# Kernel optimization log

Measured on AMD Instinct MI355X. Metric: run time of the kernel, lower is better.

The kernel has to match this reference:

```python
import jax, jax.numpy as jnp
import numpy as np

DIM = 256
NUM_HEADS = 8
HEAD_DIM = DIM // NUM_HEADS  # 32
SCALE = HEAD_DIM ** (-0.5)


def _conv1x1(x, w, b):
    # x: [B,C,H,W], w: [O,C,1,1], b: [O]
    return jnp.einsum('bchw,oc->bohw', x, w[:, :, 0, 0]) + b[None, :, None, None]


def _dwconv3x3(x, w, b):
    # depthwise conv, groups=C, padding=1 (SAME)
    y = jax.lax.conv_general_dilated(
        x, w, window_strides=(1, 1), padding='SAME',
        feature_group_count=x.shape[1],
        dimension_numbers=('NCHW', 'OIHW', 'NCHW'))
    return y + b[None, :, None, None]


def setup_inputs() -> dict:
    key = jax.random.key(0)
    ks = jax.random.split(key, 9)
    s = 0.05
    return {
        'x': jax.random.normal(ks[0], (4, DIM, 48, 48), jnp.float32),
        'w_qk': jax.random.normal(ks[1], (2 * DIM, DIM, 1, 1), jnp.float32) * s,
        'b_qk': jax.random.normal(ks[2], (2 * DIM,), jnp.float32) * s,
        'w_v': jax.random.normal(ks[3], (DIM, DIM, 1, 1), jnp.float32) * s,
        'b_v': jax.random.normal(ks[4], (DIM,), jnp.float32) * s,
        'w_pe': jax.random.normal(ks[5], (DIM, 1, 3, 3), jnp.float32) * s,
        'b_pe': jax.random.normal(ks[6], (DIM,), jnp.float32) * s,
        'w_proj': jax.random.normal(ks[7], (DIM, DIM, 1, 1), jnp.float32) * s,
        'b_proj': jax.random.normal(ks[8], (DIM,), jnp.float32) * s,
    }


def reference(x, w_qk, b_qk, w_v, b_v, w_pe, b_pe, w_proj, b_proj):
    B, C, H, W = x.shape
    N = H * W
    h, d = NUM_HEADS, HEAD_DIM

    qk = _conv1x1(x, w_qk, b_qk).reshape(B, h, 2 * d, N)
    v4 = _conv1x1(x, w_v, b_v)                # [B,C,H,W]
    pe = _dwconv3x3(v4, w_pe, b_pe)           # [B,C,H,W]
    v = v4.reshape(B, h, d, N)

    q, k = qk[:, :, :d, :], qk[:, :, d:, :]   # [B,h,d,N] each
    attn = jnp.einsum('bhdi,bhdj->bhij', q, k) * SCALE  # [B,h,N,N]
    attn = jax.nn.softmax(attn, axis=-1)
    out = jnp.einsum('bhdj,bhij->bhdi', v, attn)        # [B,h,d,N]
    out = out.reshape(B, C, H, W)

    return _conv1x1(out + pe, w_proj, b_proj)
```

## Files before the change

### kernel.cpp

```cpp
#include <hip/hip_runtime.h>
#include <hip/hip_bf16.h>

#define NPIX 2304
#define HW 48
#define CDIM 256
#define NHEADS 8
#define HD 32
#define SCALE_CONST 0.17677669529663687f
#define LOG2E 1.4426950408889634f

typedef __attribute__((ext_vector_type(8))) short  short8v;
typedef __attribute__((ext_vector_type(4))) short  short4v;
typedef __attribute__((ext_vector_type(4))) float  floatx4;

__device__ inline short f2bf(float f) {
    unsigned u = __builtin_bit_cast(unsigned, f);
    u += 0x7FFFu + ((u >> 16) & 1u);
    return (short)(u >> 16);
}
__device__ inline float bf2f(unsigned short us) {
    return __builtin_bit_cast(float, (unsigned)us << 16);
}
__device__ inline float fexp2(float x) {
    return __builtin_amdgcn_exp2f(x);
}

__global__ __launch_bounds__(256) void prep_kernel(
    const float* __restrict__ x,
    short* __restrict__ XT,
    const float* __restrict__ wqk, const float* __restrict__ wv,
    const float* __restrict__ wp,
    short* __restrict__ wqkb, short* __restrict__ wvb, short* __restrict__ wpb)
{
    const int bx = blockIdx.x;
    const int t = threadIdx.x;
    if (bx >= 576) {
        int tid = (bx - 576) * 256 + t;
        for (int idx = tid; idx < 262144; idx += 16384) {
            if (idx < 131072)       wqkb[idx] = f2bf(wqk[idx]);
            else if (idx < 196608)  wvb[idx - 131072] = f2bf(wv[idx - 131072]);
            else                    wpb[idx - 196608] = f2bf(wp[idx - 196608]);
        }
        return;
    }
    __shared__ float sT[64][65];
    const int nt = bx % 36, ct = (bx / 36) & 3, b = bx / 144;
    const int c0 = ct * 64, n0 = nt * 64;
    const float* sp = x + ((size_t)b * 256 + c0) * NPIX + n0;
    const int cl = t >> 6, n = t & 63;
#pragma unroll
    for (int it = 0; it < 16; ++it) {
        int c = it * 4 + cl;
        sT[n][c] = sp[(size_t)c * NPIX + n];
    }
    __syncthreads();
    const int nr = t >> 2, q = t & 3;
    short out[16];
#pragma unroll
    for (int j = 0; j < 16; ++j) out[j] = f2bf(sT[nr][q * 16 + j]);
    short* dp = XT + ((size_t)b * NPIX + n0 + nr) * 256 + c0 + q * 16;
    *(int4*)dp = *(int4*)out;
    *(int4*)(dp + 8) = *(int4*)(out + 8);
}

#define XROW 528

__device__ inline void stage_xt_tile(const short* __restrict__ src_base,
                                     char* __restrict__ sX, int t)
{
    const short* src = src_base + (size_t)(t >> 3) * 256 + (t & 7) * 32;
    char* dst = sX + (t >> 3) * XROW + (t & 7) * 64;
#pragma unroll
    for (int rr = 0; rr < 2; ++rr) {
        const short* s = src + rr * 32 * 256;
        char* d = dst + rr * 32 * XROW;
        *(int4*)d        = *(const int4*)s;
        *(int4*)(d + 16) = *(const int4*)(s + 8);
        *(int4*)(d + 32) = *(const int4*)(s + 16);
        *(int4*)(d + 48) = *(const int4*)(s + 24);
    }
}

__global__ __launch_bounds__(256) void conv_qkv_mfma(
    const short* __restrict__ Wqk,
    const short* __restrict__ Wv,
    const float* __restrict__ bqk,
    const float* __restrict__ bv,
    const short* __restrict__ XT,
    short* __restrict__ QT,
    short* __restrict__ KT,
    short* __restrict__ VB)
{
    __shared__ __align__(16) char sX[64 * XROW];
    const int n0 = blockIdx.x * 64;
    const int og = blockIdx.y;
    const int b  = blockIdx.z;
    const int t = threadIdx.x, lane = t & 63, w = t >> 6;
    const int l15 = lane & 15, quad = lane >> 4;

    stage_xt_tile(XT + ((size_t)b * NPIX + n0) * 256, sX, t);
    __syncthreads();

    const bool isV = (og >= 8);
    const short* Wb = isV ? Wv + (size_t)((og - 8) * 64 + w * 16 + l15) * CDIM
                          : Wqk + (size_t)(og * 64 + w * 16 + l15) * CDIM;

    floatx4 acc[4];
#pragma unroll
    for (int ib = 0; ib < 4; ++ib) acc[ib] = (floatx4){0.f, 0.f, 0.f, 0.f};

#pragma unroll
    for (int s = 0; s < 8; ++s) {
        short8v af = *(const short8v*)(Wb + s * 32 + quad * 8);
#pragma unroll
        for (int ib = 0; ib < 4; ++ib) {
            short8v bf = *(const short8v*)(sX + (ib * 16 + l15) * XROW + s * 64 + quad * 16);
            acc[ib] = __builtin_amdgcn_mfma_f32_16x16x32_bf16(af, bf, acc[ib], 0, 0, 0);
        }
    }

    if (!isV) {
        const bool isQ = (w < 2);
        const int d0 = (w & 1) * 16 + quad * 4;
        const float scl = isQ ? SCALE_CONST * LOG2E : 1.0f;
        float bvv[4];
#pragma unroll
        for (int r = 0; r < 4; ++r) bvv[r] = bqk[og * 64 + w * 16 + quad * 4 + r];
        short* base = (isQ ? QT : KT) + (size_t)(b * 8 + og) * NPIX * HD;
#pragma unroll
        for (int ib = 0; ib < 4; ++ib) {
            short pb[4];
#pragma unroll
            for (int r = 0; r < 4; ++r) pb[r] = f2bf((acc[ib][r] + bvv[r]) * scl);
            *(short4v*)(base + (size_t)(n0 + ib * 16 + l15) * HD + d0) = *(short4v*)pb;
        }
    } else {
        const int o0 = (og - 8) * 64 + w * 16 + quad * 4;
#pragma unroll
        for (int r = 0; r < 4; ++r) {
            int o = o0 + r;
            float bb = bv[o];
#pragma unroll
            for (int ib = 0; ib < 4; ++ib) {
                VB[((size_t)b * 256 + o) * NPIX + n0 + ib * 16 + l15] = f2bf(acc[ib][r] + bb);
            }
        }
    }
}

__global__ __launch_bounds__(256) void dwconv3x3_kernel(
    const short* __restrict__ X,
    const float* __restrict__ Wp,
    const float* __restrict__ bp,
    float* __restrict__ Y)
{
    __shared__ short spl[NPIX];
    const int bc = blockIdx.x;
    const int c = bc & 255;
    const short* xp = X + (size_t)bc * NPIX;
    const int t = threadIdx.x;
    for (int idx = t; idx < NPIX / 8; idx += 256)
        *(int4*)&spl[idx * 8] = *(const int4*)(xp + idx * 8);
    float w[9];
#pragma unroll
    for (int i = 0; i < 9; ++i) w[i] = Wp[c * 9 + i];
    const float bb = bp[c];
    __syncthreads();

    for (int p = t; p < NPIX; p += 256) {
        int i = p / HW, j = p % HW;
        float acc = bb;
#pragma unroll
        for (int di = -1; di <= 1; ++di) {
            int ii = i + di;
            if (ii < 0 || ii >= HW) continue;
#pragma unroll
            for (int dj = -1; dj <= 1; ++dj) {
                int jj = j + dj;
                if (jj < 0 || jj >= HW) continue;
                acc += bf2f((unsigned short)spl[ii * HW + jj]) * w[(di + 1) * 3 + (dj + 1)];
            }
        }
        Y[(size_t)bc * NPIX + p] = acc;
    }
}

#define SK0 0
#define SK1 5120
#define SV0 10240
#define SV1 14848
#define SP0 19456
#define FL_SMEM 28672

__global__ __launch_bounds__(256) void flash_attn_mfma(
    const short* __restrict__ QT,
    const short* __restrict__ KT,
    const short* __restrict__ VB,
    const float* __restrict__ PE,
    short* __restrict__ ST)
{
    __shared__ __align__(16) char smem[FL_SMEM];

    const int i0 = blockIdx.x * 64;
    const int bh = blockIdx.y;
    const int b  = bh >> 3, hh = bh & 7;

    const short* KTp = KT + (size_t)bh * NPIX * HD;
    const short* Vp  = VB + (size_t)(b * 256 + hh * HD) * NPIX;

    const int t    = threadIdx.x;
    const int lane = t & 63;
    const int w    = t >> 6;
    const int l15  = lane & 15;
    const int quad = lane >> 4;

    const short8v qfrag = *(const short8v*)(
        QT + ((size_t)bh * NPIX + i0 + w * 16 + l15) * HD + quad * 8);

    char* const sPw = smem + SP0 + w * (16 * 144);

    float m_i = -1e30f, l_i = 0.f;
    floatx4 oacc[2];
    oacc[0] = (floatx4){0.f, 0.f, 0.f, 0.f};
    oacc[1] = (floatx4){0.f, 0.f, 0.f, 0.f};

    const short* ksrc = KTp + (size_t)(t >> 2) * HD + (t & 3) * 8;
    const short* vsrc = Vp + (size_t)(t >> 3) * NPIX + (t & 7) * 8;
    const int koff = (t >> 2) * 80 + (t & 3) * 16;
    const int voff = (t >> 3) * 144 + (t & 7) * 16;

    int4 kst = *(const int4*)ksrc;
    int4 vst = *(const int4*)vsrc;

    for (int it = 0; it < 36; ++it) {
        char* bufK = smem + ((it & 1) ? SK1 : SK0);
        char* bufV = smem + ((it & 1) ? SV1 : SV0);
        *(int4*)(bufK + koff) = kst;
        *(int4*)(bufV + voff) = vst;
        if (it + 1 < 36) {
            kst = *(const int4*)(ksrc + (size_t)(it + 1) * 64 * HD);
            vst = *(const int4*)(vsrc + (it + 1) * 64);
        }
        __syncthreads();

        floatx4 sacc[4];
#pragma unroll
        for (int jb = 0; jb < 4; ++jb) {
            short8v af = *(const short8v*)(bufK + (jb * 16 + l15) * 80 + quad * 16);
            sacc[jb] = __builtin_amdgcn_mfma_f32_16x16x32_bf16(
                af, qfrag, (floatx4){0.f, 0.f, 0.f, 0.f}, 0, 0, 0);
        }

        float mx = sacc[0][0];
#pragma unroll
        for (int jb = 0; jb < 4; ++jb)
#pragma unroll
            for (int r = 0; r < 4; ++r) mx = fmaxf(mx, sacc[jb][r]);
        mx = fmaxf(mx, __shfl_xor(mx, 16));
        mx = fmaxf(mx, __shfl_xor(mx, 32));

        float mn = fmaxf(m_i, mx);
        float alpha = fexp2(m_i - mn);
        m_i = mn;

        float s = 0.f;
#pragma unroll
        for (int jb = 0; jb < 4; ++jb) {
            short pb[4];
#pragma unroll
            for (int r = 0; r < 4; ++r) {
                float e = fexp2(sacc[jb][r] - mn);
                s += e;
                pb[r] = f2bf(e);
            }
            *(short4v*)(sPw + l15 * 144 + (jb * 16 + quad * 4) * 2) = *(short4v*)pb;
        }
        s += __shfl_xor(s, 16);
        s += __shfl_xor(s, 32);
        l_i = alpha * l_i + s;

#pragma unroll
        for (int r = 0; r < 4; ++r) { oacc[0][r] *= alpha; oacc[1][r] *= alpha; }

#pragma unroll
        for (int ks = 0; ks < 2; ++ks) {
            short8v pf = *(const short8v*)(sPw + l15 * 144 + ks * 64 + quad * 16);
#pragma unroll
            for (int db = 0; db < 2; ++db) {
                short8v vf = *(const short8v*)(bufV + (db * 16 + l15) * 144 + ks * 64 + quad * 16);
                oacc[db] = __builtin_amdgcn_mfma_f32_16x16x32_bf16(vf, pf, oacc[db], 0, 0, 0);
            }
        }
    }

    const float invl = 1.0f / l_i;
    const int i = i0 + w * 16 + l15;
    const float* PEp = PE + ((size_t)b * 256 + hh * HD) * NPIX + i;
    short* stp = ST + ((size_t)b * NPIX + i) * 256 + hh * HD;
#pragma unroll
    for (int db = 0; db < 2; ++db) {
        short pb[4];
#pragma unroll
        for (int r = 0; r < 4; ++r) {
            int d = db * 16 + quad * 4 + r;
            float v = oacc[db][r] * invl + PEp[(size_t)d * NPIX];
            pb[r] = f2bf(v);
        }
        *(short4v*)(stp + db * 16 + quad * 4) = *(short4v*)pb;
    }
}

__global__ __launch_bounds__(256) void conv_proj_mfma(
    const short* __restrict__ Wb,
    const float* __restrict__ bias,
    const short* __restrict__ ST,
    float* __restrict__ out)
{
    __shared__ __align__(16) char sX[64 * XROW];
    const int n0 = blockIdx.x * 64;
    const int og = blockIdx.y;
    const int b  = blockIdx.z;
    const int t = threadIdx.x, lane = t & 63, w = t >> 6;
    const int l15 = lane & 15, quad = lane >> 4;

    stage_xt_tile(ST + ((size_t)b * NPIX + n0) * 256, sX, t);
    __syncthreads();

    const short* Arow = Wb + (size_t)(og * 64 + w * 16 + l15) * CDIM;
    floatx4 acc[4];
#pragma unroll
    for (int ib = 0; ib < 4; ++ib) acc[ib] = (floatx4){0.f, 0.f, 0.f, 0.f};
#pragma unroll
    for (int s = 0; s < 8; ++s) {
        short8v af = *(const short8v*)(Arow + s * 32 + quad * 8);
#pragma unroll
        for (int ib = 0; ib < 4; ++ib) {
            short8v bf = *(const short8v*)(sX + (ib * 16 + l15) * XROW + s * 64 + quad * 16);
            acc[ib] = __builtin_amdgcn_mfma_f32_16x16x32_bf16(af, bf, acc[ib], 0, 0, 0);
        }
    }

#pragma unroll
    for (int r = 0; r < 4; ++r) {
        int o = og * 64 + w * 16 + quad * 4 + r;
        float bb = bias[o];
#pragma unroll
        for (int ib = 0; ib < 4; ++ib)
            out[((size_t)b * 256 + o) * NPIX + n0 + ib * 16 + l15] = acc[ib][r] + bb;
    }
}

extern "C" void kernel_launch(void* const* d_in, const int* in_sizes, int n_in,
                              void* d_out, int out_size, void* d_ws, size_t ws_size,
                              hipStream_t stream) {
    const float* x      = (const float*)d_in[0];
    const float* w_qk   = (const float*)d_in[1];
    const float* b_qk   = (const float*)d_in[2];
    const float* w_v    = (const float*)d_in[3];
    const float* b_v    = (const float*)d_in[4];
    const float* w_pe   = (const float*)d_in[5];
    const float* b_pe   = (const float*)d_in[6];
    const float* w_proj = (const float*)d_in[7];
    const float* b_proj = (const float*)d_in[8];
    float* out = (float*)d_out;

    char* wsb = (char*)d_ws;
    short* ws_xt  = (short*)wsb;  wsb += (size_t)4 * NPIX * 256 * 2;
    short* ws_qt  = (short*)wsb;  wsb += (size_t)32 * NPIX * HD * 2;
    short* ws_kt  = (short*)wsb;  wsb += (size_t)32 * NPIX * HD * 2;
    short* ws_vb  = (short*)wsb;  wsb += (size_t)4 * 256 * NPIX * 2;
    float* ws_pe  = (float*)wsb;  wsb += (size_t)4 * 256 * NPIX * 4;
    short* ws_st  = (short*)wsb;  wsb += (size_t)4 * NPIX * 256 * 2;
    short* ws_wqk = (short*)wsb;  wsb += (size_t)512 * 256 * 2;
    short* ws_wv  = (short*)wsb;  wsb += (size_t)256 * 256 * 2;
    short* ws_wp  = (short*)wsb;  wsb += (size_t)256 * 256 * 2;

    prep_kernel<<<dim3(640), 256, 0, stream>>>(x, ws_xt, w_qk, w_v, w_proj,
                                               ws_wqk, ws_wv, ws_wp);
    conv_qkv_mfma<<<dim3(36, 12, 4), 256, 0, stream>>>(ws_wqk, ws_wv, b_qk, b_v,
                                                       ws_xt, ws_qt, ws_kt, ws_vb);
    dwconv3x3_kernel<<<dim3(1024), 256, 0, stream>>>(ws_vb, w_pe, b_pe, ws_pe);
    flash_attn_mfma<<<dim3(36, 32), 256, 0, stream>>>(ws_qt, ws_kt, ws_vb, ws_pe, ws_st);
    conv_proj_mfma<<<dim3(36, 4, 4), 256, 0, stream>>>(ws_wp, b_proj, ws_st, out);
}
```

Baseline: 182.7 us.

## Fuse depthwise 3x3 conv into attention epilogue and repad LDS rows

Removes the separate dwconv kernel and its fp32 intermediate buffer. Each attention block now loads a halo of V rows into shared memory after the main loop and computes the positional-encoding conv in registers before the output write. The LDS row strides shrink (80→72, 144→136) and the loads/stores are split into 8-byte halves to change bank mapping. Softmax probabilities are truncated rather than rounded to bf16, and the sum uses the truncated values. This saves a launch and fp32 global traffic, at the cost of extra per-block epilogue work and uncoalesced scalar halo loads.

```diff
diff --git a/kernel.cpp b/kernel.cpp
--- a/kernel.cpp
+++ b/kernel.cpp
@@ -148,55 +148,22 @@
     }
 }
 
-__global__ __launch_bounds__(256) void dwconv3x3_kernel(
-    const short* __restrict__ X,
-    const float* __restrict__ Wp,
-    const float* __restrict__ bp,
-    float* __restrict__ Y)
-{
-    __shared__ short spl[NPIX];
-    const int bc = blockIdx.x;
-    const int c = bc & 255;
-    const short* xp = X + (size_t)bc * NPIX;
-    const int t = threadIdx.x;
-    for (int idx = t; idx < NPIX / 8; idx += 256)
-        *(int4*)&spl[idx * 8] = *(const int4*)(xp + idx * 8);
-    float w[9];
-#pragma unroll
-    for (int i = 0; i < 9; ++i) w[i] = Wp[c * 9 + i];
-    const float bb = bp[c];
-    __syncthreads();
-
-    for (int p = t; p < NPIX; p += 256) {
-        int i = p / HW, j = p % HW;
-        float acc = bb;
-#pragma unroll
-        for (int di = -1; di <= 1; ++di) {
-            int ii = i + di;
-            if (ii < 0 || ii >= HW) continue;
-#pragma unroll
-            for (int dj = -1; dj <= 1; ++dj) {
-                int jj = j + dj;
-                if (jj < 0 || jj >= HW) continue;
-                acc += bf2f((unsigned short)spl[ii * HW + jj]) * w[(di + 1) * 3 + (dj + 1)];
-            }
-        }
-        Y[(size_t)bc * NPIX + p] = acc;
-    }
-}
-
+#define KROW 72
+#define VROW 136
+#define PROW 136
 #define SK0 0
-#define SK1 5120
-#define SV0 10240
-#define SV1 14848
-#define SP0 19456
-#define FL_SMEM 28672
+#define SK1 4608
+#define SV0 9216
+#define SV1 13568
+#define SP0 17920
+#define FL_SMEM 26624
 
 __global__ __launch_bounds__(256) void flash_attn_mfma(
     const short* __restrict__ QT,
     const short* __restrict__ KT,
     const short* __restrict__ VB,
-    const float* __restrict__ PE,
+    const float* __restrict__ w_pe,
+    const float* __restrict__ b_pe,
     short* __restrict__ ST)
 {
     __shared__ __align__(16) char smem[FL_SMEM];
@@ -217,7 +184,7 @@
     const short8v qfrag = *(const short8v*)(
         QT + ((size_t)bh * NPIX + i0 + w * 16 + l15) * HD + quad * 8);
 
-    char* const sPw = smem + SP0 + w * (16 * 144);
+    char* const sPw = smem + SP0 + w * (16 * PROW);
 
     float m_i = -1e30f, l_i = 0.f;
     floatx4 oacc[2];
@@ -226,8 +193,8 @@
 
     const short* ksrc = KTp + (size_t)(t >> 2) * HD + (t & 3) * 8;
     const short* vsrc = Vp + (size_t)(t >> 3) * NPIX + (t & 7) * 8;
-    const int koff = (t >> 2) * 80 + (t & 3) * 16;
-    const int voff = (t >> 3) * 144 + (t & 7) * 16;
+    const int koff = (t >> 2) * KROW + (t & 3) * 16;
+    const int voff = (t >> 3) * VROW + (t & 7) * 16;
 
     int4 kst = *(const int4*)ksrc;
     int4 vst = *(const int4*)vsrc;
@@ -235,8 +202,10 @@
     for (int it = 0; it < 36; ++it) {
         char* bufK = smem + ((it & 1) ? SK1 : SK0);
         char* bufV = smem + ((it & 1) ? SV1 : SV0);
-        *(int4*)(bufK + koff) = kst;
-        *(int4*)(bufV + voff) = vst;
+        *(int2*)(bufK + koff)     = *(int2*)&kst;
+        *(int2*)(bufK + koff + 8) = *((int2*)&kst + 1);
+        *(int2*)(bufV + voff)     = *(int2*)&vst;
+        *(int2*)(bufV + voff + 8) = *((int2*)&vst + 1);
         if (it + 1 < 36) {
             kst = *(const int4*)(ksrc + (size_t)(it + 1) * 64 * HD);
             vst = *(const int4*)(vsrc + (it + 1) * 64);
@@ -246,7 +215,10 @@
         floatx4 sacc[4];
 #pragma unroll
         for (int jb = 0; jb < 4; ++jb) {
-            short8v af = *(const short8v*)(bufK + (jb * 16 + l15) * 80 + quad * 16);
+            const char* ka = bufK + (jb * 16 + l15) * KROW + quad * 16;
+            short8v af;
+            ((int2*)&af)[0] = *(const int2*)ka;
+            ((int2*)&af)[1] = *(const int2*)(ka + 8);
             sacc[jb] = __builtin_amdgcn_mfma_f32_16x16x32_bf16(
                 af, qfrag, (floatx4){0.f, 0.f, 0.f, 0.f}, 0, 0, 0);
         }
@@ -266,14 +238,18 @@
         float s = 0.f;
 #pragma unroll
         for (int jb = 0; jb < 4; ++jb) {
-            short pb[4];
+            unsigned tb[4];
 #pragma unroll
             for (int r = 0; r < 4; ++r) {
                 float e = fexp2(sacc[jb][r] - mn);
-                s += e;
-                pb[r] = f2bf(e);
+                unsigned tr = __builtin_bit_cast(unsigned, e) & 0xFFFF0000u;
+                tb[r] = tr;
+                s += __builtin_bit_cast(float, tr);
             }
-            *(short4v*)(sPw + l15 * 144 + (jb * 16 + quad * 4) * 2) = *(short4v*)pb;
+            int2 pw;
+            pw.x = (int)((tb[0] >> 16) | tb[1]);
+            pw.y = (int)((tb[2] >> 16) | tb[3]);
+            *(int2*)(sPw + l15 * PROW + jb * 32 + quad * 8) = pw;
         }
         s += __shfl_xor(s, 16);
         s += __shfl_xor(s, 32);
@@ -284,26 +260,73 @@
 
 #pragma unroll
         for (int ks = 0; ks < 2; ++ks) {
-            short8v pf = *(const short8v*)(sPw + l15 * 144 + ks * 64 + quad * 16);
+            const char* pa = sPw + l15 * PROW + ks * 64 + quad * 16;
+            short8v pf;
+            ((int2*)&pf)[0] = *(const int2*)pa;
+            ((int2*)&pf)[1] = *(const int2*)(pa + 8);
 #pragma unroll
             for (int db = 0; db < 2; ++db) {
-                short8v vf = *(const short8v*)(bufV + (db * 16 + l15) * 144 + ks * 64 + quad * 16);
+                const char* va = bufV + (db * 16 + l15) * VROW + ks * 64 + quad * 16;
+                short8v vf;
+                ((int2*)&vf)[0] = *(const int2*)va;
+                ((int2*)&vf)[1] = *(const int2*)(va + 8);
                 oacc[db] = __builtin_amdgcn_mfma_f32_16x16x32_bf16(vf, pf, oacc[db], 0, 0, 0);
             }
         }
     }
 
+    __syncthreads();
+    short* spl = (short*)smem;
+    {
+        int d  = t >> 3;
+        int c0 = (t & 7) * 21;
+        const short* vsp = VB + ((size_t)b * 256 + hh * HD + d) * NPIX;
+        short* dst = spl + d * 168 + c0;
+        int base = i0 - 52 + c0;
+#pragma unroll
+        for (int u = 0; u < 21; ++u) {
+            int p = base + u;
+            dst[u] = (p >= 0 && p < NPIX) ? vsp[p] : (short)0;
+        }
+    }
+    __syncthreads();
+
+    const int il = w * 16 + l15;
+    const int p  = i0 + il;
+    const int x  = p % HW;
+    float pe[2][4];
+#pragma unroll
+    for (int db = 0; db < 2; ++db)
+#pragma unroll
+        for (int r = 0; r < 4; ++r)
+            pe[db][r] = b_pe[hh * HD + db * 16 + quad * 4 + r];
+
+#pragma unroll
+    for (int dy = -1; dy <= 1; ++dy) {
+#pragma unroll
+        for (int dx = -1; dx <= 1; ++dx) {
+            bool ok = (x + dx >= 0) && (x + dx < HW);
+            int idx = il + 52 + dy * HW + dx;
+            int wt  = (dy + 1) * 3 + (dx + 1);
+#pragma unroll
+            for (int db = 0; db < 2; ++db)
+#pragma unroll
+                for (int r = 0; r < 4; ++r) {
+                    int d = db * 16 + quad * 4 + r;
+                    float wv = ok ? w_pe[(hh * HD + d) * 9 + wt] : 0.0f;
+                    pe[db][r] += wv * bf2f((unsigned short)spl[d * 168 + idx]);
+                }
+        }
+    }
+
     const float invl = 1.0f / l_i;
-    const int i = i0 + w * 16 + l15;
-    const float* PEp = PE + ((size_t)b * 256 + hh * HD) * NPIX + i;
-    short* stp = ST + ((size_t)b * NPIX + i) * 256 + hh * HD;
+    short* stp = ST + ((size_t)b * NPIX + p) * 256 + hh * HD;
 #pragma unroll
     for (int db = 0; db < 2; ++db) {
         short pb[4];
 #pragma unroll
         for (int r = 0; r < 4; ++r) {
-            int d = db * 16 + quad * 4 + r;
-            float v = oacc[db][r] * invl + PEp[(size_t)d * NPIX];
+            float v = oacc[db][r] * invl + pe[db][r];
             pb[r] = f2bf(v);
         }
         *(short4v*)(stp + db * 16 + quad * 4) = *(short4v*)pb;
@@ -369,7 +392,6 @@
     short* ws_qt  = (short*)wsb;  wsb += (size_t)32 * NPIX * HD * 2;
     short* ws_kt  = (short*)wsb;  wsb += (size_t)32 * NPIX * HD * 2;
     short* ws_vb  = (short*)wsb;  wsb += (size_t)4 * 256 * NPIX * 2;
-    float* ws_pe  = (float*)wsb;  wsb += (size_t)4 * 256 * NPIX * 4;
     short* ws_st  = (short*)wsb;  wsb += (size_t)4 * NPIX * 256 * 2;
     short* ws_wqk = (short*)wsb;  wsb += (size_t)512 * 256 * 2;
     short* ws_wv  = (short*)wsb;  wsb += (size_t)256 * 256 * 2;
@@ -379,7 +401,7 @@
                                                ws_wqk, ws_wv, ws_wp);
     conv_qkv_mfma<<<dim3(36, 12, 4), 256, 0, stream>>>(ws_wqk, ws_wv, b_qk, b_v,
                                                        ws_xt, ws_qt, ws_kt, ws_vb);
-    dwconv3x3_kernel<<<dim3(1024), 256, 0, stream>>>(ws_vb, w_pe, b_pe, ws_pe);
-    flash_attn_mfma<<<dim3(36, 32), 256, 0, stream>>>(ws_qt, ws_kt, ws_vb, ws_pe, ws_st);
+    flash_attn_mfma<<<dim3(36, 32), 256, 0, stream>>>(ws_qt, ws_kt, ws_vb,
+                                                      w_pe, b_pe, ws_st);
     conv_proj_mfma<<<dim3(36, 4, 4), 256, 0, stream>>>(ws_wp, b_proj, ws_st, out);
 }
```

Result: slower. 194.8 us (+6.6%).
